# Kernel optimization log

Measured on AMD Instinct MI355X. Metric: run time of the kernel, lower is better.

Reference implementation:

```python
import jax, jax.numpy as jnp
import numpy as np

B, T, S, D, H, FF = 4, 1024, 1024, 1024, 16, 4096
DH = D // H
NEG = -1e9
EPS = 1e-5


def setup_inputs() -> dict:
    key = jax.random.key(0)
    ks = jax.random.split(key, 20)
    p = 0.02  # param init scale
    inp = {
        "x": jax.random.normal(ks[0], (B, T, D), jnp.float32),
        "encoder_output": jax.random.normal(ks[1], (B, S, D), jnp.float32),
        "src_mask": jnp.ones((B, 1, 1, S), jnp.bool_),
        "tgt_mask": jnp.tril(jnp.ones((1, 1, T, T), jnp.bool_)),  # causal
        # self-attention params
        "d_Wq": jax.random.normal(ks[2], (D, D)) * p, "d_bq": jnp.zeros((D,)),
        "d_Wk": jax.random.normal(ks[3], (D, D)) * p, "d_bk": jnp.zeros((D,)),
        "d_Wv": jax.random.normal(ks[4], (D, D)) * p, "d_bv": jnp.zeros((D,)),
        "d_Wo": jax.random.normal(ks[5], (D, D)) * p, "d_bo": jnp.zeros((D,)),
        # cross-attention params
        "e_Wq": jax.random.normal(ks[6], (D, D)) * p, "e_bq": jnp.zeros((D,)),
        "e_Wk": jax.random.normal(ks[7], (D, D)) * p, "e_bk": jnp.zeros((D,)),
        "e_Wv": jax.random.normal(ks[8], (D, D)) * p, "e_bv": jnp.zeros((D,)),
        "e_Wo": jax.random.normal(ks[9], (D, D)) * p, "e_bo": jnp.zeros((D,)),
        # FFN params
        "ff_W1": jax.random.normal(ks[10], (D, FF)) * p, "ff_b1": jnp.zeros((FF,)),
        "ff_W2": jax.random.normal(ks[11], (FF, D)) * p, "ff_b2": jnp.zeros((D,)),
        # layernorm params
        "ln1_g": jnp.ones((D,)), "ln1_b": jnp.zeros((D,)),
        "ln2_g": jnp.ones((D,)), "ln2_b": jnp.zeros((D,)),
        "ln3_g": jnp.ones((D,)), "ln3_b": jnp.zeros((D,)),
    }
    return inp


def _mha(xq, xkv, Wq, bq, Wk, bk, Wv, bv, Wo, bo, mask):
    b, tq = xq.shape[0], xq.shape[1]
    q = (xq @ Wq + bq).reshape(b, tq, H, DH).transpose(0, 2, 1, 3)
    k = (xkv @ Wk + bk).reshape(b, -1, H, DH).transpose(0, 2, 1, 3)
    v = (xkv @ Wv + bv).reshape(b, -1, H, DH).transpose(0, 2, 1, 3)
    scores = jnp.einsum("bhqd,bhkd->bhqk", q, k) / np.float32(np.sqrt(DH))
    scores = jnp.where(mask, scores, NEG)
    attn = jax.nn.softmax(scores, axis=-1)
    out = jnp.einsum("bhqk,bhkd->bhqd", attn, v)
    out = out.transpose(0, 2, 1, 3).reshape(b, tq, D)
    return out @ Wo + bo


def _ln(x, g, b):
    m = jnp.mean(x, axis=-1, keepdims=True)
    v = jnp.var(x, axis=-1, keepdims=True)
    return (x - m) / jnp.sqrt(v + EPS) * g + b


def reference(x, encoder_output, src_mask, tgt_mask,
              d_Wq, d_bq, d_Wk, d_bk, d_Wv, d_bv, d_Wo, d_bo,
              e_Wq, e_bq, e_Wk, e_bk, e_Wv, e_bv, e_Wo, e_bo,
              ff_W1, ff_b1, ff_W2, ff_b2,
              ln1_g, ln1_b, ln2_g, ln2_b, ln3_g, ln3_b):
    # masked self-attention + residual + LN (dropout is identity in eval)
    d = _mha(x, x, d_Wq, d_bq, d_Wk, d_bk, d_Wv, d_bv, d_Wo, d_bo, tgt_mask)
    d = _ln(d + x, ln1_g, ln1_b)
    # cross-attention over encoder output + residual + LN
    f = _mha(d, encoder_output, e_Wq, e_bq, e_Wk, e_bk, e_Wv, e_bv, e_Wo, e_bo, src_mask)
    f = _ln(f + d, ln2_g, ln2_b)
    # FFN + residual + LN
    g = jax.nn.relu(f @ ff_W1 + ff_b1) @ ff_W2 + ff_b2
    g = _ln(g + f, ln3_g, ln3_b)
    return g
```

## Files before the change

kernel.cpp:

```cpp
#include <hip/hip_runtime.h>

static constexpr int Bc = 4, Tc = 1024, Sc = 1024, Dc = 1024, Hc = 16, DHc = 64, FFc = 4096;

typedef __attribute__((ext_vector_type(8))) short short8;
typedef __attribute__((ext_vector_type(4))) short short4v;
typedef __attribute__((ext_vector_type(4))) float f32x4;

__device__ __forceinline__ unsigned short f2bf(float f) {
    unsigned int u = __float_as_uint(f);
    unsigned int r = u + 0x7fffu + ((u >> 16) & 1u);
    return (unsigned short)(r >> 16);
}
__device__ __forceinline__ float bf2f(unsigned short u) {
    return __uint_as_float(((unsigned int)u) << 16);
}

__device__ __forceinline__ void gload_lds16(const void* g, void* l) {
    __builtin_amdgcn_global_load_lds((const __attribute__((address_space(1))) void*)g,
                                     (__attribute__((address_space(3))) void*)l, 16, 0, 0);
}

__global__ __launch_bounds__(256) void cast_f32_bf16(const float* __restrict__ in,
                                                     unsigned short* __restrict__ out, int n8) {
    int i = blockIdx.x * 256 + threadIdx.x;
    if (i >= n8) return;
    const float4* p = (const float4*)in + (size_t)i * 2;
    float4 a = p[0], b = p[1];
    short8 o;
    o[0] = f2bf(a.x); o[1] = f2bf(a.y); o[2] = f2bf(a.z); o[3] = f2bf(a.w);
    o[4] = f2bf(b.x); o[5] = f2bf(b.y); o[6] = f2bf(b.z); o[7] = f2bf(b.w);
    *(short8*)(out + (size_t)i * 8) = o;
}

__global__ __launch_bounds__(256) void transpose_cast(const float* __restrict__ W,
                                                      unsigned short* __restrict__ Wt,
                                                      int K, int N) {
    __shared__ float tile[32][33];
    int n0 = blockIdx.x * 32, k0 = blockIdx.y * 32;
    int tx = threadIdx.x, ty = threadIdx.y;
#pragma unroll
    for (int i = 0; i < 4; i++)
        tile[ty + i * 8][tx] = W[(size_t)(k0 + ty + i * 8) * N + n0 + tx];
    __syncthreads();
#pragma unroll
    for (int i = 0; i < 4; i++)
        Wt[(size_t)(n0 + ty + i * 8) * K + k0 + tx] = f2bf(tile[tx][ty + i * 8]);
}

struct TP8 { const float* s[8]; unsigned short* d[8]; };
__global__ __launch_bounds__(256) void transpose_cast8(TP8 p) {
    __shared__ float tile[32][33];
    const float* W = p.s[blockIdx.z];
    unsigned short* Wt = p.d[blockIdx.z];
    int n0 = blockIdx.x * 32, k0 = blockIdx.y * 32;
    int tx = threadIdx.x, ty = threadIdx.y;
#pragma unroll
    for (int i = 0; i < 4; i++)
        tile[ty + i * 8][tx] = W[(size_t)(k0 + ty + i * 8) * 1024 + n0 + tx];
    __syncthreads();
#pragma unroll
    for (int i = 0; i < 4; i++)
        Wt[(size_t)(n0 + ty + i * 8) * 1024 + k0 + tx] = f2bf(tile[tx][ty + i * 8]);
}

__global__ void concat_bias(const float* b0, const float* b1, const float* b2,
                            float* __restrict__ out) {
    int i = blockIdx.x * 256 + threadIdx.x;
    int seg = i >> 10, j = i & 1023;
    const float* p = seg == 0 ? b0 : (seg == 1 ? b1 : b2);
    out[i] = p[j];
}

__global__ __launch_bounds__(256) void transpose_v(const unsigned short* __restrict__ V, int ldv,
                                                   unsigned short* __restrict__ Vt) {
    __shared__ unsigned short t[64 * 64];
    const int bh = blockIdx.y, b = bh >> 4, h = bh & 15;
    const int s0 = blockIdx.x * 64;
    const int tid = threadIdx.x;
    const int r = tid >> 2, ch = tid & 3;
    const unsigned short* src = V + (size_t)(b * 1024 + s0 + r) * ldv + h * 64 + ch * 16;
    short8 v0 = *(const short8*)src;
    short8 v1 = *(const short8*)(src + 8);
    int pw_ = (ch ^ r ^ (r >> 4)) & 3;
    *(short8*)(t + r * 64 + pw_ * 16) = v0;
    *(short8*)(t + r * 64 + pw_ * 16 + 8) = v1;
    __syncthreads();
    const int dh = tid >> 2, sc = (tid & 3) * 16;
    short8 o0, o1;
#pragma unroll
    for (int j = 0; j < 8; j++) {
        int c0 = sc + j, c1 = sc + 8 + j;
        o0[j] = t[c0 * 64 + (((dh >> 4) ^ c0 ^ (c0 >> 4)) & 3) * 16 + (dh & 15)];
        o1[j] = t[c1 * 64 + (((dh >> 4) ^ c1 ^ (c1 >> 4)) & 3) * 16 + (dh & 15)];
    }
    unsigned short* dst = Vt + ((size_t)bh * 64 + dh) * 1024 + s0 + sc;
    *(short8*)dst = o0;
    *(short8*)(dst + 8) = o1;
}

template <int EPI>
__global__ __launch_bounds__(256) void gemm_db(const unsigned short* __restrict__ A,
                                               const unsigned short* __restrict__ Bt,
                                               const float* __restrict__ bias,
                                               float* __restrict__ outF,
                                               unsigned short* __restrict__ outB,
                                               int M, int N, int Kloop, int lda, int ldb) {
    __shared__ unsigned short As[2][128 * 32];
    __shared__ unsigned short Bs[2][128 * 32];
    const int tid = threadIdx.x;
    const int w = tid >> 6, lane = tid & 63, l4 = lane & 15, g = lane >> 4;
    const int m0 = blockIdx.y * 128, n0 = blockIdx.x * 128;
    const int z = blockIdx.z;
    A += (size_t)z * Kloop;
    Bt += (size_t)z * Kloop;
    const int wr = w >> 1, wc = w & 1;
    f32x4 acc[4][4] = {};
    const int r0 = tid >> 2;
    const int kk = ((tid & 3) ^ ((tid >> 3) & 3)) * 8;
    const int sk = (l4 >> 1) & 3;
    gload_lds16(A + (size_t)(m0 + r0) * lda + kk, (char*)As[0] + tid * 16);
    gload_lds16(A + (size_t)(m0 + 64 + r0) * lda + kk, (char*)As[0] + 4096 + tid * 16);
    gload_lds16(Bt + (size_t)(n0 + r0) * ldb + kk, (char*)Bs[0] + tid * 16);
    gload_lds16(Bt + (size_t)(n0 + 64 + r0) * ldb + kk, (char*)Bs[0] + 4096 + tid * 16);
    __syncthreads();
    int buf = 0;
    for (int k0 = 0; k0 < Kloop; k0 += 32) {
        if (k0 + 32 < Kloop) {
            const int kn = k0 + 32;
            gload_lds16(A + (size_t)(m0 + r0) * lda + kn + kk, (char*)As[buf ^ 1] + tid * 16);
            gload_lds16(A + (size_t)(m0 + 64 + r0) * lda + kn + kk, (char*)As[buf ^ 1] + 4096 + tid * 16);
            gload_lds16(Bt + (size_t)(n0 + r0) * ldb + kn + kk, (char*)Bs[buf ^ 1] + tid * 16);
            gload_lds16(Bt + (size_t)(n0 + 64 + r0) * ldb + kn + kk, (char*)Bs[buf ^ 1] + 4096 + tid * 16);
        }
        short8 a[4], b[4];
#pragma unroll
        for (int m = 0; m < 4; m++)
            a[m] = *(const short8*)(As[buf] + (wr * 64 + m * 16 + l4) * 32 + (g ^ sk) * 8);
#pragma unroll
        for (int n = 0; n < 4; n++)
            b[n] = *(const short8*)(Bs[buf] + (wc * 64 + n * 16 + l4) * 32 + (g ^ sk) * 8);
#pragma unroll
        for (int m = 0; m < 4; m++)
#pragma unroll
            for (int n = 0; n < 4; n++)
                acc[m][n] = __builtin_amdgcn_mfma_f32_16x16x32_bf16(a[m], b[n], acc[m][n], 0, 0, 0);
        __syncthreads();
        buf ^= 1;
    }
    const int rowB = m0 + wr * 64 + g * 4;
    const int colB = n0 + wc * 64 + l4;
    float* oF = (EPI == 1) ? outF + (size_t)z * M * N : outF;
#pragma unroll
    for (int n = 0; n < 4; n++) {
        float bv = (EPI == 1 && z != 0) ? 0.f : bias[colB + n * 16];
#pragma unroll
        for (int m = 0; m < 4; m++) {
#pragma unroll
            for (int r = 0; r < 4; r++) {
                float v = acc[m][n][r] + bv;
                if (EPI == 2) v = fmaxf(v, 0.f);
                size_t idx = (size_t)(rowB + m * 16 + r) * N + colB + n * 16;
                if (EPI == 1) oF[idx] = v;
                else outB[idx] = f2bf(v);
            }
        }
    }
}

template <int EPI>
__global__ __launch_bounds__(256) void gemm64_db(const unsigned short* __restrict__ A,
                                                 const unsigned short* __restrict__ Bt,
                                                 const float* __restrict__ bias,
                                                 float* __restrict__ outF,
                                                 unsigned short* __restrict__ outB,
                                                 int M, int N, int Kloop, int lda, int ldb) {
    __shared__ unsigned short As[2][64 * 32];
    __shared__ unsigned short Bs[2][128 * 32];
    const int tid = threadIdx.x;
    const int w = tid >> 6, lane = tid & 63, l4 = lane & 15, g = lane >> 4;
    const int m0 = blockIdx.y * 64, n0 = blockIdx.x * 128;
    f32x4 acc[4][2] = {};
    const int r0 = tid >> 2;
    const int kk = ((tid & 3) ^ ((tid >> 3) & 3)) * 8;
    const int sk = (l4 >> 1) & 3;
    gload_lds16(A + (size_t)(m0 + r0) * lda + kk, (char*)As[0] + tid * 16);
    gload_lds16(Bt + (size_t)(n0 + r0) * ldb + kk, (char*)Bs[0] + tid * 16);
    gload_lds16(Bt + (size_t)(n0 + 64 + r0) * ldb + kk, (char*)Bs[0] + 4096 + tid * 16);
    __syncthreads();
    int buf = 0;
    for (int k0 = 0; k0 < Kloop; k0 += 32) {
        if (k0 + 32 < Kloop) {
            const int kn = k0 + 32;
            gload_lds16(A + (size_t)(m0 + r0) * lda + kn + kk, (char*)As[buf ^ 1] + tid * 16);
            gload_lds16(Bt + (size_t)(n0 + r0) * ldb + kn + kk, (char*)Bs[buf ^ 1] + tid * 16);
            gload_lds16(Bt + (size_t)(n0 + 64 + r0) * ldb + kn + kk, (char*)Bs[buf ^ 1] + 4096 + tid * 16);
        }
        short8 a[4], b[2];
#pragma unroll
        for (int m = 0; m < 4; m++)
            a[m] = *(const short8*)(As[buf] + (m * 16 + l4) * 32 + (g ^ sk) * 8);
#pragma unroll
        for (int n = 0; n < 2; n++)
            b[n] = *(const short8*)(Bs[buf] + (w * 32 + n * 16 + l4) * 32 + (g ^ sk) * 8);
#pragma unroll
        for (int m = 0; m < 4; m++)
#pragma unroll
            for (int n = 0; n < 2; n++)
                acc[m][n] = __builtin_amdgcn_mfma_f32_16x16x32_bf16(a[m], b[n], acc[m][n], 0, 0, 0);
        __syncthreads();
        buf ^= 1;
    }
    const int rowB = m0 + g * 4;
    const int colB = n0 + w * 32 + l4;
#pragma unroll
    for (int n = 0; n < 2; n++) {
        float bv = bias[colB + n * 16];
#pragma unroll
        for (int m = 0; m < 4; m++) {
#pragma unroll
            for (int r = 0; r < 4; r++) {
                float v = acc[m][n][r] + bv;
                if (EPI == 2) v = fmaxf(v, 0.f);
                size_t idx = (size_t)(rowB + m * 16 + r) * N + colB + n * 16;
                if (EPI == 1) outF[idx] = v;
                else outB[idx] = f2bf(v);
            }
        }
    }
}

template <int CAUSAL>
__global__ __launch_bounds__(256) void attn4_kernel(const unsigned short* __restrict__ Q, int ldq,
                                                    const unsigned short* __restrict__ Kg, int ldk,
                                                    const unsigned short* __restrict__ Vt,
                                                    unsigned short* __restrict__ O) {
    __shared__ unsigned short Kl[2 * 64 * 64];
    __shared__ unsigned short Vl[2 * 64 * 64];
    __shared__ unsigned short Pl[4][16 * 72];
    const int bh = blockIdx.x, qb = blockIdx.y;
    const int b = bh >> 4, h = bh & 15;
    const int tid = threadIdx.x, w = tid >> 6, lane = tid & 63;
    const int l4 = lane & 15, g = lane >> 4;
    const int q0 = qb * 64 + w * 16;
    const unsigned short* Qp = Q + (size_t)(b * Tc + q0 + l4) * ldq + h * DHc + g * 8;
    short8 qf0 = *(const short8*)Qp;
    short8 qf1 = *(const short8*)(Qp + 32);
    const unsigned short* Kbase = Kg + (size_t)(b * 1024) * ldk + h * DHc;
    const unsigned short* Vbase = Vt + (size_t)bh * DHc * 1024;
    f32x4 o[4] = {};
    float mrun = -1e30f, lrun = 0.f;
    const int nT = CAUSAL ? qb + 1 : 16;
    unsigned short* pw = &Pl[w][l4 * 72];
    const int qi = q0 + l4;

    const int sr0 = tid >> 3;
    const int sr1 = 32 + sr0;
    const int sc_ = (tid & 7) ^ (sr0 & 7);

    auto stage = [&](int s0, int buf) {
        char* kd = (char*)Kl + buf * 8192;
        char* vd = (char*)Vl + buf * 8192;
        gload_lds16(Kbase + (size_t)(s0 + sr0) * ldk + sc_ * 8, kd + tid * 16);
        gload_lds16(Kbase + (size_t)(s0 + sr1) * ldk + sc_ * 8, kd + 4096 + tid * 16);
        gload_lds16(Vbase + (size_t)sr0 * 1024 + s0 + sc_ * 8, vd + tid * 16);
        gload_lds16(Vbase + (size_t)sr1 * 1024 + s0 + sc_ * 8, vd + 4096 + tid * 16);
    };

    stage(0, 0);
    __syncthreads();
    int buf = 0;
    const int sw = l4 & 7;

    for (int t = 0; t < nT; ++t) {
        const int s0 = t * 64;
        if (t + 1 < nT) stage(s0 + 64, buf ^ 1);
        const unsigned short* Kb_ = Kl + buf * 4096;
        const unsigned short* Vb_ = Vl + buf * 4096;
        f32x4 st[4];
        f32x4 z = {0.f, 0.f, 0.f, 0.f};
        __builtin_amdgcn_s_setprio(1);
#pragma unroll
        for (int c = 0; c < 4; c++) {
            const unsigned short* kr = Kb_ + (c * 16 + l4) * 64;
            short8 ka0 = *(const short8*)(kr + ((g ^ sw) * 8));
            short8 ka1 = *(const short8*)(kr + (((g + 4) ^ sw) * 8));
            st[c] = __builtin_amdgcn_mfma_f32_16x16x32_bf16(ka0, qf0, z, 0, 0, 0);
            st[c] = __builtin_amdgcn_mfma_f32_16x16x32_bf16(ka1, qf1, st[c], 0, 0, 0);
        }
        __builtin_amdgcn_s_setprio(0);
        float p[16];
        float tmax = -1e30f;
        const bool domask = CAUSAL && (t == nT - 1);
#pragma unroll
        for (int c = 0; c < 4; c++)
#pragma unroll
            for (int r = 0; r < 4; r++) {
                float v = st[c][r] * 0.125f;
                if (domask && (s0 + c * 16 + g * 4 + r) > qi) v = -1e9f;
                p[c * 4 + r] = v;
                tmax = fmaxf(tmax, v);
            }
        tmax = fmaxf(tmax, __shfl_xor(tmax, 16));
        tmax = fmaxf(tmax, __shfl_xor(tmax, 32));
        if (!__all(tmax <= mrun + 8.f)) {
            float mnew = fmaxf(mrun, tmax);
            float al = __expf(mrun - mnew);
            lrun *= al;
#pragma unroll
            for (int d = 0; d < 4; d++) o[d] *= al;
            mrun = mnew;
        }
        float ps = 0.f;
#pragma unroll
        for (int i = 0; i < 16; i++) { p[i] = __expf(p[i] - mrun); ps += p[i]; }
        ps += __shfl_xor(ps, 16);
        ps += __shfl_xor(ps, 32);
        lrun += ps;
#pragma unroll
        for (int c = 0; c < 4; c++) {
            short4v pk;
            pk[0] = f2bf(p[c * 4 + 0]); pk[1] = f2bf(p[c * 4 + 1]);
            pk[2] = f2bf(p[c * 4 + 2]); pk[3] = f2bf(p[c * 4 + 3]);
            *(short4v*)(pw + c * 16 + g * 4) = pk;
        }
        short8 pb_lo = *(const short8*)(pw + g * 8);
        short8 pb_hi = *(const short8*)(pw + 32 + g * 8);
        __builtin_amdgcn_s_setprio(1);
#pragma unroll
        for (int d = 0; d < 4; d++) {
            const unsigned short* vr = Vb_ + (d * 16 + l4) * 64;
            short8 va0 = *(const short8*)(vr + ((g ^ sw) * 8));
            short8 va1 = *(const short8*)(vr + (((g + 4) ^ sw) * 8));
            o[d] = __builtin_amdgcn_mfma_f32_16x16x32_bf16(va0, pb_lo, o[d], 0, 0, 0);
            o[d] = __builtin_amdgcn_mfma_f32_16x16x32_bf16(va1, pb_hi, o[d], 0, 0, 0);
        }
        __builtin_amdgcn_s_setprio(0);
        __syncthreads();
        buf ^= 1;
    }
    float inv = 1.f / lrun;
    unsigned short* Ob = O + (size_t)(b * Tc + q0 + l4) * Dc + h * DHc;
#pragma unroll
    for (int d = 0; d < 4; d++) {
#pragma unroll
        for (int r = 0; r < 4; r++) Ob[d * 16 + g * 4 + r] = f2bf(o[d][r] * inv);
    }
}

__global__ __launch_bounds__(256) void ln_bf(const unsigned short* __restrict__ a,
                                             const unsigned short* __restrict__ res,
                                             const float* __restrict__ gam,
                                             const float* __restrict__ bet,
                                             unsigned short* __restrict__ outB,
                                             float* __restrict__ outF) {
    int row = blockIdx.x, t = threadIdx.x;
    size_t base = (size_t)row * Dc + t * 4;
    short4v av = *(const short4v*)(a + base);
    short4v rv = *(const short4v*)(res + base);
    float x0 = bf2f((unsigned short)av[0]) + bf2f((unsigned short)rv[0]);
    float x1 = bf2f((unsigned short)av[1]) + bf2f((unsigned short)rv[1]);
    float x2 = bf2f((unsigned short)av[2]) + bf2f((unsigned short)rv[2]);
    float x3 = bf2f((unsigned short)av[3]) + bf2f((unsigned short)rv[3]);
    float s = x0 + x1 + x2 + x3;
    float ss = x0 * x0 + x1 * x1 + x2 * x2 + x3 * x3;
    for (int o = 1; o < 64; o <<= 1) { s += __shfl_xor(s, o); ss += __shfl_xor(ss, o); }
    __shared__ float S1[4], S2[4];
    int w = t >> 6;
    if ((t & 63) == 0) { S1[w] = s; S2[w] = ss; }
    __syncthreads();
    s = S1[0] + S1[1] + S1[2] + S1[3];
    ss = S2[0] + S2[1] + S2[2] + S2[3];
    float mean = s * (1.f / Dc);
    float var = ss * (1.f / Dc) - mean * mean;
    float rstd = rsqrtf(var + 1e-5f);
    int c = t * 4;
    float4 g4 = *(const float4*)(gam + c);
    float4 b4 = *(const float4*)(bet + c);
    float y0 = (x0 - mean) * rstd * g4.x + b4.x;
    float y1 = (x1 - mean) * rstd * g4.y + b4.y;
    float y2 = (x2 - mean) * rstd * g4.z + b4.z;
    float y3 = (x3 - mean) * rstd * g4.w + b4.w;
    if (outB) {
        short4v ob;
        ob[0] = f2bf(y0); ob[1] = f2bf(y1); ob[2] = f2bf(y2); ob[3] = f2bf(y3);
        *(short4v*)(outB + base) = ob;
    }
    if (outF) { float4 ov = {y0, y1, y2, y3}; *(float4*)(outF + base) = ov; }
}

__global__ __launch_bounds__(256) void ln_2f(const float* __restrict__ a0,
                                             const float* __restrict__ a1,
                                             const unsigned short* __restrict__ res,
                                             const float* __restrict__ gam,
                                             const float* __restrict__ bet,
                                             unsigned short* __restrict__ outB,
                                             float* __restrict__ outF) {
    int row = blockIdx.x, t = threadIdx.x;
    size_t base = (size_t)row * Dc + t * 4;
    float4 u = *(const float4*)(a0 + base);
    float4 v = *(const float4*)(a1 + base);
    short4v rv = *(const short4v*)(res + base);
    float x0 = u.x + v.x + bf2f((unsigned short)rv[0]);
    float x1 = u.y + v.y + bf2f((unsigned short)rv[1]);
    float x2 = u.z + v.z + bf2f((unsigned short)rv[2]);
    float x3 = u.w + v.w + bf2f((unsigned short)rv[3]);
    float s = x0 + x1 + x2 + x3;
    float ss = x0 * x0 + x1 * x1 + x2 * x2 + x3 * x3;
    for (int o = 1; o < 64; o <<= 1) { s += __shfl_xor(s, o); ss += __shfl_xor(ss, o); }
    __shared__ float S1[4], S2[4];
    int w = t >> 6;
    if ((t & 63) == 0) { S1[w] = s; S2[w] = ss; }
    __syncthreads();
    s = S1[0] + S1[1] + S1[2] + S1[3];
    ss = S2[0] + S2[1] + S2[2] + S2[3];
    float mean = s * (1.f / Dc);
    float var = ss * (1.f / Dc) - mean * mean;
    float rstd = rsqrtf(var + 1e-5f);
    int c = t * 4;
    float4 g4 = *(const float4*)(gam + c);
    float4 b4 = *(const float4*)(bet + c);
    float y0 = (x0 - mean) * rstd * g4.x + b4.x;
    float y1 = (x1 - mean) * rstd * g4.y + b4.y;
    float y2 = (x2 - mean) * rstd * g4.z + b4.z;
    float y3 = (x3 - mean) * rstd * g4.w + b4.w;
    if (outB) {
        short4v ob;
        ob[0] = f2bf(y0); ob[1] = f2bf(y1); ob[2] = f2bf(y2); ob[3] = f2bf(y3);
        *(short4v*)(outB + base) = ob;
    }
    if (outF) { float4 ov = {y0, y1, y2, y3}; *(float4*)(outF + base) = ov; }
}

extern "C" void kernel_launch(void* const* d_in, const int* in_sizes, int n_in,
                              void* d_out, int out_size, void* d_ws, size_t ws_size,
                              hipStream_t stream) {
    const float* x   = (const float*)d_in[0];
    const float* enc = (const float*)d_in[1];
    const float* dWq = (const float*)d_in[4];  const float* dbq = (const float*)d_in[5];
    const float* dWk = (const float*)d_in[6];  const float* dbk = (const float*)d_in[7];
    const float* dWv = (const float*)d_in[8];  const float* dbv = (const float*)d_in[9];
    const float* dWo = (const float*)d_in[10]; const float* dbo = (const float*)d_in[11];
    const float* eWq = (const float*)d_in[12]; const float* ebq = (const float*)d_in[13];
    const float* eWk = (const float*)d_in[14]; const float* ebk = (const float*)d_in[15];
    const float* eWv = (const float*)d_in[16]; const float* ebv = (const float*)d_in[17];
    const float* eWo = (const float*)d_in[18]; const float* ebo = (const float*)d_in[19];
    const float* fW1 = (const float*)d_in[20]; const float* fb1 = (const float*)d_in[21];
    const float* fW2 = (const float*)d_in[22]; const float* fb2 = (const float*)d_in[23];
    const float* g1 = (const float*)d_in[24];  const float* be1 = (const float*)d_in[25];
    const float* g2 = (const float*)d_in[26];  const float* be2 = (const float*)d_in[27];
    const float* g3 = (const float*)d_in[28];  const float* be3 = (const float*)d_in[29];

    char* ws = (char*)d_ws;
    size_t off = 0;
    auto alloc = [&](size_t bytes) -> void* {
        void* p = ws + off;
        off += (bytes + 255) & ~(size_t)255;
        return p;
    };
    const size_t A = (size_t)4096 * 1024;
    const size_t MB1 = (size_t)1024 * 1024;
    char* R1 = (char*)alloc(32 * 1024 * 1024);
    unsigned short* qkv = (unsigned short*)R1;
    unsigned short* kvx = (unsigned short*)R1;
    unsigned short* qx  = (unsigned short*)(R1 + 16 * 1024 * 1024);
    unsigned short* h1  = (unsigned short*)R1;
    unsigned short* xb   = (unsigned short*)alloc(A * 2);
    unsigned short* encb = (unsigned short*)alloc(A * 2);
    unsigned short* wqkv = (unsigned short*)alloc(3 * MB1 * 2);
    unsigned short* wekv = (unsigned short*)alloc(2 * MB1 * 2);
    unsigned short* weq  = (unsigned short*)alloc(MB1 * 2);
    unsigned short* wdo  = (unsigned short*)alloc(MB1 * 2);
    unsigned short* weo  = (unsigned short*)alloc(MB1 * 2);
    unsigned short* wf1  = (unsigned short*)alloc(4 * MB1 * 2);
    unsigned short* wf2  = (unsigned short*)alloc(4 * MB1 * 2);
    float* bqkv = (float*)alloc(3072 * 4);
    float* bekv = (float*)alloc(2048 * 4);
    unsigned short* VtB = (unsigned short*)alloc(A * 2);
    unsigned short* ab  = (unsigned short*)alloc(A * 2);
    unsigned short* tmpB = (unsigned short*)alloc(A * 2);
    unsigned short* dB = (unsigned short*)alloc(A * 2);
    unsigned short* fB = (unsigned short*)alloc(A * 2);
    float* pf0 = (float*)VtB;
    float* pf1 = pf0 + A;
    (void)ws_size; (void)in_sizes; (void)n_in; (void)out_size;

    dim3 tb(32, 8);
    cast_f32_bf16<<<2048, 256, 0, stream>>>(x, xb, (int)(A / 8));
    cast_f32_bf16<<<2048, 256, 0, stream>>>(enc, encb, (int)(A / 8));
    TP8 tp;
    tp.s[0] = dWq; tp.d[0] = wqkv;
    tp.s[1] = dWk; tp.d[1] = wqkv + MB1;
    tp.s[2] = dWv; tp.d[2] = wqkv + 2 * MB1;
    tp.s[3] = eWk; tp.d[3] = wekv;
    tp.s[4] = eWv; tp.d[4] = wekv + MB1;
    tp.s[5] = eWq; tp.d[5] = weq;
    tp.s[6] = dWo; tp.d[6] = wdo;
    tp.s[7] = eWo; tp.d[7] = weo;
    transpose_cast8<<<dim3(32, 32, 8), tb, 0, stream>>>(tp);
    transpose_cast<<<dim3(128, 32), tb, 0, stream>>>(fW1, wf1, 1024, 4096);
    transpose_cast<<<dim3(32, 128), tb, 0, stream>>>(fW2, wf2, 4096, 1024);
    concat_bias<<<12, 256, 0, stream>>>(dbq, dbk, dbv, bqkv);
    concat_bias<<<8, 256, 0, stream>>>(ebk, ebv, ebv, bekv);

    gemm_db<0><<<dim3(24, 32, 1), 256, 0, stream>>>(xb, wqkv, bqkv, nullptr, qkv, 4096, 3072, 1024, 1024, 1024);
    transpose_v<<<dim3(16, 64), 256, 0, stream>>>(qkv + 2048, 3072, VtB);
    attn4_kernel<1><<<dim3(64, 16), 256, 0, stream>>>(qkv, 3072, qkv + 1024, 3072, VtB, ab);
    gemm64_db<0><<<dim3(8, 64), 256, 0, stream>>>(ab, wdo, dbo, nullptr, tmpB, 4096, 1024, 1024, 1024, 1024);
    ln_bf<<<4096, 256, 0, stream>>>(tmpB, xb, g1, be1, dB, nullptr);

    gemm_db<0><<<dim3(16, 32, 1), 256, 0, stream>>>(encb, wekv, bekv, nullptr, kvx, 4096, 2048, 1024, 1024, 1024);
    gemm64_db<0><<<dim3(8, 64), 256, 0, stream>>>(dB, weq, ebq, nullptr, qx, 4096, 1024, 1024, 1024, 1024);
    transpose_v<<<dim3(16, 64), 256, 0, stream>>>(kvx + 1024, 2048, VtB);
    attn4_kernel<0><<<dim3(64, 16), 256, 0, stream>>>(qx, 1024, kvx, 2048, VtB, ab);
    gemm64_db<0><<<dim3(8, 64), 256, 0, stream>>>(ab, weo, ebo, nullptr, tmpB, 4096, 1024, 1024, 1024, 1024);
    ln_bf<<<4096, 256, 0, stream>>>(tmpB, dB, g2, be2, fB, nullptr);

    gemm_db<2><<<dim3(32, 32, 1), 256, 0, stream>>>(fB, wf1, fb1, nullptr, h1, 4096, 4096, 1024, 1024, 1024);
    gemm_db<1><<<dim3(8, 32, 2), 256, 0, stream>>>(h1, wf2, fb2, pf0, nullptr, 4096, 1024, 2048, 4096, 4096);
    ln_2f<<<4096, 256, 0, stream>>>(pf0, pf1, fB, g3, be3, nullptr, (float*)d_out);
}
```

Before: 373.1 us.

## Triple-buffer GEMM LDS pipeline and remap blocks for XCD/L2 locality

Both GEMM kernels move from a double-buffered to a triple-buffered LDS pipeline. Loads run two K-steps ahead, and partial vmcnt waits plus raw barriers replace the full __syncthreads. Block indices are also remapped so consecutive workgroups on the same XCD (flat id mod 8) cover grouped column tiles, which should improve L2 reuse. The extra buffer raises LDS use per block and may cut occupancy. The vmcnt counts depend on the compiler issuing no other outstanding memory ops.

```diff
diff --git a/kernel.cpp b/kernel.cpp
--- a/kernel.cpp
+++ b/kernel.cpp
@@ -98,6 +98,25 @@
     *(short8*)(dst + 8) = o1;
 }
 
+struct BlkMap { int m, n, z; };
+__device__ __forceinline__ BlkMap remap_block() {
+    const int gx = gridDim.x, gy = gridDim.y;
+    const int nxy = gx * gy;
+    const int nwg = nxy * gridDim.z;
+    const int flat = (blockIdx.z * gy + blockIdx.y) * gx + blockIdx.x;
+    const int id = (flat & 7) * (nwg >> 3) + (flat >> 3);
+    const int pz = id / nxy;
+    const int rz = id - pz * nxy;
+    const int gsz = 8 * gy;
+    const int grp = rz / gsz;
+    const int rem = rz - grp * gsz;
+    BlkMap r;
+    r.m = rem >> 3;
+    r.n = grp * 8 + (rem & 7);
+    r.z = pz;
+    return r;
+}
+
 template <int EPI>
 __global__ __launch_bounds__(256) void gemm_db(const unsigned short* __restrict__ A,
                                                const unsigned short* __restrict__ Bt,
@@ -105,12 +124,12 @@
                                                float* __restrict__ outF,
                                                unsigned short* __restrict__ outB,
                                                int M, int N, int Kloop, int lda, int ldb) {
-    __shared__ unsigned short As[2][128 * 32];
-    __shared__ unsigned short Bs[2][128 * 32];
+    __shared__ unsigned short As[3][128 * 32];
+    __shared__ unsigned short Bs[3][128 * 32];
     const int tid = threadIdx.x;
     const int w = tid >> 6, lane = tid & 63, l4 = lane & 15, g = lane >> 4;
-    const int m0 = blockIdx.y * 128, n0 = blockIdx.x * 128;
-    const int z = blockIdx.z;
+    BlkMap bm = remap_block();
+    const int m0 = bm.m * 128, n0 = bm.n * 128, z = bm.z;
     A += (size_t)z * Kloop;
     Bt += (size_t)z * Kloop;
     const int wr = w >> 1, wc = w & 1;
@@ -118,19 +137,27 @@
     const int r0 = tid >> 2;
     const int kk = ((tid & 3) ^ ((tid >> 3) & 3)) * 8;
     const int sk = (l4 >> 1) & 3;
-    gload_lds16(A + (size_t)(m0 + r0) * lda + kk, (char*)As[0] + tid * 16);
-    gload_lds16(A + (size_t)(m0 + 64 + r0) * lda + kk, (char*)As[0] + 4096 + tid * 16);
-    gload_lds16(Bt + (size_t)(n0 + r0) * ldb + kk, (char*)Bs[0] + tid * 16);
-    gload_lds16(Bt + (size_t)(n0 + 64 + r0) * ldb + kk, (char*)Bs[0] + 4096 + tid * 16);
-    __syncthreads();
+    const unsigned short* Ar0 = A + (size_t)(m0 + r0) * lda + kk;
+    const unsigned short* Ar1 = A + (size_t)(m0 + 64 + r0) * lda + kk;
+    const unsigned short* Br0 = Bt + (size_t)(n0 + r0) * ldb + kk;
+    const unsigned short* Br1 = Bt + (size_t)(n0 + 64 + r0) * ldb + kk;
+    auto stage = [&](int sb, int k0) {
+        gload_lds16(Ar0 + k0, (char*)As[sb] + tid * 16);
+        gload_lds16(Ar1 + k0, (char*)As[sb] + 4096 + tid * 16);
+        gload_lds16(Br0 + k0, (char*)Bs[sb] + tid * 16);
+        gload_lds16(Br1 + k0, (char*)Bs[sb] + 4096 + tid * 16);
+    };
+    const int nk = Kloop >> 5;
+    stage(0, 0);
+    stage(1, 32);
+    asm volatile("s_waitcnt vmcnt(4)" ::: "memory");
+    __builtin_amdgcn_s_barrier();
+    asm volatile("" ::: "memory");
     int buf = 0;
-    for (int k0 = 0; k0 < Kloop; k0 += 32) {
-        if (k0 + 32 < Kloop) {
-            const int kn = k0 + 32;
-            gload_lds16(A + (size_t)(m0 + r0) * lda + kn + kk, (char*)As[buf ^ 1] + tid * 16);
-            gload_lds16(A + (size_t)(m0 + 64 + r0) * lda + kn + kk, (char*)As[buf ^ 1] + 4096 + tid * 16);
-            gload_lds16(Bt + (size_t)(n0 + r0) * ldb + kn + kk, (char*)Bs[buf ^ 1] + tid * 16);
-            gload_lds16(Bt + (size_t)(n0 + 64 + r0) * ldb + kn + kk, (char*)Bs[buf ^ 1] + 4096 + tid * 16);
+    for (int t = 0; t < nk; ++t) {
+        if (t + 2 < nk) {
+            int b2 = buf + 2; if (b2 >= 3) b2 -= 3;
+            stage(b2, (t + 2) * 32);
         }
         short8 a[4], b[4];
 #pragma unroll
@@ -144,8 +171,13 @@
 #pragma unroll
             for (int n = 0; n < 4; n++)
                 acc[m][n] = __builtin_amdgcn_mfma_f32_16x16x32_bf16(a[m], b[n], acc[m][n], 0, 0, 0);
-        __syncthreads();
-        buf ^= 1;
+        if (t + 1 < nk) {
+            if (t + 2 < nk) asm volatile("s_waitcnt vmcnt(4)" ::: "memory");
+            else            asm volatile("s_waitcnt vmcnt(0)" ::: "memory");
+            __builtin_amdgcn_s_barrier();
+            asm volatile("" ::: "memory");
+        }
+        buf = (buf + 1 == 3) ? 0 : buf + 1;
     }
     const int rowB = m0 + wr * 64 + g * 4;
     const int colB = n0 + wc * 64 + l4;
@@ -174,26 +206,35 @@
                                                  float* __restrict__ outF,
                                                  unsigned short* __restrict__ outB,
                                                  int M, int N, int Kloop, int lda, int ldb) {
-    __shared__ unsigned short As[2][64 * 32];
-    __shared__ unsigned short Bs[2][128 * 32];
+    __shared__ unsigned short As[3][64 * 32];
+    __shared__ unsigned short Bs[3][128 * 32];
     const int tid = threadIdx.x;
     const int w = tid >> 6, lane = tid & 63, l4 = lane & 15, g = lane >> 4;
-    const int m0 = blockIdx.y * 64, n0 = blockIdx.x * 128;
+    BlkMap bm = remap_block();
+    const int m0 = bm.m * 64, n0 = bm.n * 128;
     f32x4 acc[4][2] = {};
     const int r0 = tid >> 2;
     const int kk = ((tid & 3) ^ ((tid >> 3) & 3)) * 8;
     const int sk = (l4 >> 1) & 3;
-    gload_lds16(A + (size_t)(m0 + r0) * lda + kk, (char*)As[0] + tid * 16);
-    gload_lds16(Bt + (size_t)(n0 + r0) * ldb + kk, (char*)Bs[0] + tid * 16);
-    gload_lds16(Bt + (size_t)(n0 + 64 + r0) * ldb + kk, (char*)Bs[0] + 4096 + tid * 16);
-    __syncthreads();
+    const unsigned short* Ar0 = A + (size_t)(m0 + r0) * lda + kk;
+    const unsigned short* Br0 = Bt + (size_t)(n0 + r0) * ldb + kk;
+    const unsigned short* Br1 = Bt + (size_t)(n0 + 64 + r0) * ldb + kk;
+    auto stage = [&](int sb, int k0) {
+        gload_lds16(Ar0 + k0, (char*)As[sb] + tid * 16);
+        gload_lds16(Br0 + k0, (char*)Bs[sb] + tid * 16);
+        gload_lds16(Br1 + k0, (char*)Bs[sb] + 4096 + tid * 16);
+    };
+    const int nk = Kloop >> 5;
+    stage(0, 0);
+    stage(1, 32);
+    asm volatile("s_waitcnt vmcnt(3)" ::: "memory");
+    __builtin_amdgcn_s_barrier();
+    asm volatile("" ::: "memory");
     int buf = 0;
-    for (int k0 = 0; k0 < Kloop; k0 += 32) {
-        if (k0 + 32 < Kloop) {
-            const int kn = k0 + 32;
-            gload_lds16(A + (size_t)(m0 + r0) * lda + kn + kk, (char*)As[buf ^ 1] + tid * 16);
-            gload_lds16(Bt + (size_t)(n0 + r0) * ldb + kn + kk, (char*)Bs[buf ^ 1] + tid * 16);
-            gload_lds16(Bt + (size_t)(n0 + 64 + r0) * ldb + kn + kk, (char*)Bs[buf ^ 1] + 4096 + tid * 16);
+    for (int t = 0; t < nk; ++t) {
+        if (t + 2 < nk) {
+            int b2 = buf + 2; if (b2 >= 3) b2 -= 3;
+            stage(b2, (t + 2) * 32);
         }
         short8 a[4], b[2];
 #pragma unroll
@@ -207,8 +248,13 @@
 #pragma unroll
             for (int n = 0; n < 2; n++)
                 acc[m][n] = __builtin_amdgcn_mfma_f32_16x16x32_bf16(a[m], b[n], acc[m][n], 0, 0, 0);
-        __syncthreads();
-        buf ^= 1;
+        if (t + 1 < nk) {
+            if (t + 2 < nk) asm volatile("s_waitcnt vmcnt(3)" ::: "memory");
+            else            asm volatile("s_waitcnt vmcnt(0)" ::: "memory");
+            __builtin_amdgcn_s_barrier();
+            asm volatile("" ::: "memory");
+        }
+        buf = (buf + 1 == 3) ? 0 : buf + 1;
     }
     const int rowB = m0 + g * 4;
     const int colB = n0 + w * 32 + l4;
```

Result: faster. 365.5 us (-2.0%).
